# Kernel optimization log

Hardware: AMD Instinct MI355X
Metric: run time of the kernel (lower is better)

## Reference

```python
import jax, jax.numpy as jnp
import numpy as np

N_NODES = 50000
N_EDGES = 800000
D = 128


def _gcn_norm(edge_index, edge_weights, n_nodes):
    # PyG gcn_norm with add_self_loops=True, fill_value=1.0
    src = jnp.concatenate([edge_index[0], jnp.arange(n_nodes)])
    dst = jnp.concatenate([edge_index[1], jnp.arange(n_nodes)])
    w = jnp.concatenate([edge_weights, jnp.ones((n_nodes,), edge_weights.dtype)])
    deg = jax.ops.segment_sum(w, dst, num_segments=n_nodes)
    dinv = jnp.where(deg > 0, jax.lax.rsqrt(deg), 0.0)
    norm = dinv[src] * w * dinv[dst]  # [E + N]
    return src, dst, norm


def _gcn_conv(x, src, dst, norm, W, b, n_nodes):
    h = x @ W                                   # [N, F_out]
    msg = h[src] * norm[:, None]                # gather + scale, [E+N, F_out]
    out = jax.ops.segment_sum(msg, dst, num_segments=n_nodes)
    return out + b


def setup_inputs() -> dict:
    key = jax.random.key(0)
    ks = jax.random.split(key, 12)
    s = 1.0 / np.sqrt(D)
    return {
        "x": jax.random.normal(ks[0], (N_NODES, D), jnp.float32),
        "edge_index": jax.random.randint(ks[1], (2, N_EDGES), 0, N_NODES, jnp.int64),
        "edge_weights": jax.random.uniform(ks[2], (N_EDGES,), jnp.float32),
        "W1": jax.random.normal(ks[3], (D, D), jnp.float32) * s,
        "b1": jnp.zeros((D,), jnp.float32),
        "W2": jax.random.normal(ks[4], (D, D), jnp.float32) * s,
        "b2": jnp.zeros((D,), jnp.float32),
        "W3": jax.random.normal(ks[5], (D, D), jnp.float32) * s,
        "b3": jnp.zeros((D,), jnp.float32),
        "Wl": jax.random.normal(ks[6], (D, D), jnp.float32) * s,
        "bl": jnp.zeros((D,), jnp.float32),
    }


def reference(x, edge_index, edge_weights, W1, b1, W2, b2, W3, b3, Wl, bl):
    n = x.shape[0]
    src, dst, norm = _gcn_norm(edge_index, edge_weights, n)
    h = _gcn_conv(x, src, dst, norm, W1, b1, n)
    h = jax.nn.relu(h)
    h = _gcn_conv(h, src, dst, norm, W2, b2, n)
    h = jax.nn.relu(h)
    h = _gcn_conv(h, src, dst, norm, W3, b3, n)
    # final 'linear' activation entry == nn.Linear(out_size, out_size)
    return h @ Wl + bl
```

## Files before the change

### kernel.cpp

```cpp
#include <hip/hip_runtime.h>
#include <hip/hip_fp16.h>


#define D 128

typedef __attribute__((ext_vector_type(8))) _Float16 half8;
typedef __attribute__((ext_vector_type(4))) float floatx4;

#define CNT_STRIDE 16

__global__ __launch_bounds__(256) void k_edge_pass1(const int* __restrict__ dst,
                                                    unsigned int* __restrict__ cntp,
                                                    int* __restrict__ loc, int E) {
    int e = blockIdx.x * 256 + threadIdx.x;
    if (e < E) {
        int d = dst[e];
        loc[e] = (int)atomicAdd(&cntp[(size_t)d * CNT_STRIDE], 1u);
    }
}

__device__ inline int block_exscan_256(int v) {
    int tid = threadIdx.x;
    int lane = tid & 63, wv = tid >> 6;
    int incl = v;
#pragma unroll
    for (int d = 1; d < 64; d <<= 1) {
        int n = __shfl_up(incl, d, 64);
        if (lane >= d) incl += n;
    }
    __shared__ int wsum[4];
    if (lane == 63) wsum[wv] = incl;
    __syncthreads();
    int woff = 0;
#pragma unroll
    for (int j = 0; j < 4; j++) woff += (j < wv) ? wsum[j] : 0;
    return woff + incl - v;
}

__global__ __launch_bounds__(256) void k_scan_a(const unsigned int* __restrict__ cntp,
                                                int* bsum, int N) {
    int i = blockIdx.x * 256 + threadIdx.x;
    int v = (i < N) ? (int)cntp[(size_t)i * CNT_STRIDE] : 0;
#pragma unroll
    for (int d = 32; d; d >>= 1) v += __shfl_down(v, d, 64);
    __shared__ int ws4[4];
    int lane = threadIdx.x & 63, wv = threadIdx.x >> 6;
    if (lane == 0) ws4[wv] = v;
    __syncthreads();
    if (threadIdx.x == 0) bsum[blockIdx.x] = ws4[0] + ws4[1] + ws4[2] + ws4[3];
}

__global__ __launch_bounds__(256) void k_scan_b(const int* __restrict__ bsum,
                                                int* boff, int nb) {
    int tid = threadIdx.x;
    int v = (tid < nb) ? bsum[tid] : 0;
    int ex = block_exscan_256(v);
    if (tid < nb) boff[tid] = ex;
}

__global__ __launch_bounds__(256) void k_scan_c(const unsigned int* __restrict__ cntp,
                                                const int* __restrict__ boff,
                                                int* rp, int N, int E) {
    int i = blockIdx.x * 256 + threadIdx.x;
    int v = (i < N) ? (int)cntp[(size_t)i * CNT_STRIDE] : 0;
    int ex = block_exscan_256(v);
    if (i < N) rp[i] = boff[blockIdx.x] + ex;
    if (i == 0) rp[N] = E;
}

__global__ __launch_bounds__(256) void k_fill(const int* __restrict__ ei,
                                              const float* __restrict__ w,
                                              const int* __restrict__ rp,
                                              const int* __restrict__ loc,
                                              unsigned int* __restrict__ ev, int E) {
    int e = blockIdx.x * 256 + threadIdx.x;
    if (e < E) {
        int s = ei[e];
        int d = ei[E + e];
        int p = rp[d] + loc[e];
        unsigned int wq = (unsigned int)__float2uint_rn(w[e] * 32767.0f);
        ev[p] = (wq << 17) | (unsigned int)s;
    }
}

__global__ __launch_bounds__(256) void k_deg(const int* __restrict__ rp,
                                             const unsigned int* __restrict__ ev,
                                             float* __restrict__ dinv, int N) {
    int i = blockIdx.x * 256 + threadIdx.x;
    if (i < N) {
        int e0 = rp[i], e1 = rp[i + 1];
        float s = 0.f;
        for (int e = e0; e < e1; e++)
            s += (float)(ev[e] >> 17);
        dinv[i] = rsqrtf(1.0f + s * (1.0f / 32767.0f));
    }
}

template <bool A_IS_F32>
__global__ __launch_bounds__(256) void k_gemm_mfma(const void* __restrict__ Aptr,
                                                   const float* __restrict__ W,
                                                   const float* __restrict__ dinv,
                                                   const float* __restrict__ bias,
                                                   float* __restrict__ C32,
                                                   __half* __restrict__ C16, int N) {
    __shared__ _Float16 Wl[128][136];
    int tid = threadIdx.x;

#pragma unroll
    for (int j = 0; j < 64; j++) {
        int e = tid + j * 256;
        int k = e >> 7, n = e & 127;
        Wl[n][k] = (_Float16)W[e];
    }
    __syncthreads();

    int wave = tid >> 6, lane = tid & 63;
    int m = lane & 15, q = lane >> 4;
    int R0 = blockIdx.x * 128 + wave * 32;

    const float*  A32p = (const float*)Aptr;
    const __half* A16p = (const __half*)Aptr;

    floatx4 acc[2][8];
#pragma unroll
    for (int rt = 0; rt < 2; rt++)
#pragma unroll
        for (int ct = 0; ct < 8; ct++) acc[rt][ct] = (floatx4){0.f, 0.f, 0.f, 0.f};

#pragma unroll
    for (int kk = 0; kk < 4; kk++) {
        half8 a[2];
#pragma unroll
        for (int rt = 0; rt < 2; rt++) {
            int row = R0 + rt * 16 + m;
            half8 t = {0, 0, 0, 0, 0, 0, 0, 0};
            if (row < N) {
                if (A_IS_F32) {
                    const float* p = &A32p[(size_t)row * 128 + kk * 32 + q * 8];
                    float4 f0 = *(const float4*)p;
                    float4 f1 = *(const float4*)(p + 4);
                    t[0] = (_Float16)f0.x; t[1] = (_Float16)f0.y;
                    t[2] = (_Float16)f0.z; t[3] = (_Float16)f0.w;
                    t[4] = (_Float16)f1.x; t[5] = (_Float16)f1.y;
                    t[6] = (_Float16)f1.z; t[7] = (_Float16)f1.w;
                } else {
                    t = *(const half8*)&A16p[(size_t)row * 128 + kk * 32 + q * 8];
                }
            }
            a[rt] = t;
        }
#pragma unroll
        for (int ct = 0; ct < 8; ct++) {
            half8 b = *(const half8*)&Wl[ct * 16 + m][kk * 32 + q * 8];
            acc[0][ct] = __builtin_amdgcn_mfma_f32_16x16x32_f16(a[0], b, acc[0][ct], 0, 0, 0);
            acc[1][ct] = __builtin_amdgcn_mfma_f32_16x16x32_f16(a[1], b, acc[1][ct], 0, 0, 0);
        }
    }

#pragma unroll
    for (int rt = 0; rt < 2; rt++) {
#pragma unroll
        for (int r = 0; r < 4; r++) {
            int row = R0 + rt * 16 + q * 4 + r;
            if (row >= N) continue;
            float dv = (dinv != nullptr) ? dinv[row] : 1.0f;
#pragma unroll
            for (int ct = 0; ct < 8; ct++) {
                int col = ct * 16 + m;
                float v = acc[rt][ct][r] * dv;
                if (C16) C16[(size_t)row * 128 + col] = __float2half_rn(v);
                if (C32) C32[(size_t)row * 128 + col] = v + bias[col];
            }
        }
    }
}

__global__ __launch_bounds__(256) void k_agg(const __half* __restrict__ y16,
                                             const int* __restrict__ rp,
                                             const unsigned int* __restrict__ ev,
                                             const float* __restrict__ dinv,
                                             const float* __restrict__ bias,
                                             __half* __restrict__ out16,
                                             int N, int relu) {
    int i = blockIdx.x * 4 + (threadIdx.x >> 6);
    if (i >= N) return;
    int lane = threadIdx.x & 63;
    int g = lane >> 4;
    int sl = lane & 15;

    float acc[8];
#pragma unroll
    for (int j = 0; j < 8; j++) acc[j] = 0.f;

    int e0 = rp[i], e1 = rp[i + 1];

    for (int e = e0; e < e1; e += 16) {
        unsigned int p[4];
        float v[4];
        uint4 q[4];
#pragma unroll
        for (int u = 0; u < 4; u++) {
            int idx = e + u * 4 + g;
            bool ok = idx < e1;
            p[u] = ev[ok ? idx : e0];
            v[u] = ok ? (float)(p[u] >> 17) * (1.0f / 32767.0f) : 0.0f;
        }
#pragma unroll
        for (int u = 0; u < 4; u++)
            q[u] = *(const uint4*)&y16[(size_t)(p[u] & 0x1FFFFu) * D + sl * 8];
#pragma unroll
        for (int u = 0; u < 4; u++) {
            union { uint4 uu; __half2 h2[4]; } U; U.uu = q[u];
            float2 f0 = __half22float2(U.h2[0]);
            float2 f1 = __half22float2(U.h2[1]);
            float2 f2 = __half22float2(U.h2[2]);
            float2 f3 = __half22float2(U.h2[3]);
            acc[0] = fmaf(v[u], f0.x, acc[0]); acc[1] = fmaf(v[u], f0.y, acc[1]);
            acc[2] = fmaf(v[u], f1.x, acc[2]); acc[3] = fmaf(v[u], f1.y, acc[3]);
            acc[4] = fmaf(v[u], f2.x, acc[4]); acc[5] = fmaf(v[u], f2.y, acc[5]);
            acc[6] = fmaf(v[u], f3.x, acc[6]); acc[7] = fmaf(v[u], f3.y, acc[7]);
        }
    }

#pragma unroll
    for (int j = 0; j < 8; j++) {
        acc[j] += __shfl_xor(acc[j], 16, 64);
        acc[j] += __shfl_xor(acc[j], 32, 64);
    }

    if (g == 0) {
        float di = dinv[i];
        union { uint4 u; __half2 h2[4]; } S;
        S.u = *(const uint4*)&y16[(size_t)i * D + sl * 8];
        float2 s0 = __half22float2(S.h2[0]);
        float2 s1 = __half22float2(S.h2[1]);
        float2 s2 = __half22float2(S.h2[2]);
        float2 s3 = __half22float2(S.h2[3]);
        float4 b0 = *(const float4*)&bias[sl * 8];
        float4 b1 = *(const float4*)&bias[sl * 8 + 4];
        float o[8];
        o[0] = b0.x + di * (acc[0] + s0.x);
        o[1] = b0.y + di * (acc[1] + s0.y);
        o[2] = b0.z + di * (acc[2] + s1.x);
        o[3] = b0.w + di * (acc[3] + s1.y);
        o[4] = b1.x + di * (acc[4] + s2.x);
        o[5] = b1.y + di * (acc[5] + s2.y);
        o[6] = b1.z + di * (acc[6] + s3.x);
        o[7] = b1.w + di * (acc[7] + s3.y);
        if (relu) {
#pragma unroll
            for (int j = 0; j < 8; j++) o[j] = fmaxf(o[j], 0.f);
        }
        union { uint4 u; __half2 h2[4]; } O;
        O.h2[0] = __float22half2_rn(make_float2(o[0], o[1]));
        O.h2[1] = __float22half2_rn(make_float2(o[2], o[3]));
        O.h2[2] = __float22half2_rn(make_float2(o[4], o[5]));
        O.h2[3] = __float22half2_rn(make_float2(o[6], o[7]));
        *(uint4*)&out16[(size_t)i * D + sl * 8] = O.u;
    }
}

extern "C" void kernel_launch(void* const* d_in, const int* in_sizes, int n_in,
                              void* d_out, int out_size, void* d_ws, size_t ws_size,
                              hipStream_t stream) {
    const float* x  = (const float*)d_in[0];
    const int*   ei = (const int*)d_in[1];
    const float* ew = (const float*)d_in[2];
    const float* W1 = (const float*)d_in[3];
    const float* b1 = (const float*)d_in[4];
    const float* W2 = (const float*)d_in[5];
    const float* b2 = (const float*)d_in[6];
    const float* W3 = (const float*)d_in[7];
    const float* b3 = (const float*)d_in[8];
    const float* Wl = (const float*)d_in[9];
    const float* bl = (const float*)d_in[10];

    int N = in_sizes[0] / D;
    int E = in_sizes[2];

    char* ws = (char*)d_ws;
    size_t off = 0;
    auto alloc = [&](size_t bytes) {
        void* p = ws + off;
        off = (off + bytes + 255) & ~(size_t)255;
        return p;
    };
    unsigned int* cntp = (unsigned int*)alloc((size_t)N * CNT_STRIDE * 4);
    float*  dinv = (float*)alloc((size_t)N * 4);
    int*    bsum = (int*)  alloc(1024);
    int*    boff = (int*)  alloc(1024);
    int*    rp   = (int*)  alloc((size_t)(N + 1) * 4);
    int*    loc  = (int*)  alloc((size_t)E * 4);
    unsigned int* ev = (unsigned int*)alloc((size_t)E * 4);
    __half* y16  = (__half*)alloc((size_t)N * D * 2);
    __half* z16  = (__half*)alloc((size_t)N * D * 2);

    int nbN = (N + 255) / 256;
    int nbE = (E + 255) / 256;

    hipMemsetAsync(cntp, 0, (size_t)N * CNT_STRIDE * 4, stream);
    k_edge_pass1<<<nbE, 256, 0, stream>>>(ei + E, cntp, loc, E);
    k_scan_a<<<nbN, 256, 0, stream>>>(cntp, bsum, N);
    k_scan_b<<<1, 256, 0, stream>>>(bsum, boff, nbN);
    k_scan_c<<<nbN, 256, 0, stream>>>(cntp, boff, rp, N, E);
    k_fill<<<nbE, 256, 0, stream>>>(ei, ew, rp, loc, ev, E);
    k_deg<<<nbN, 256, 0, stream>>>(rp, ev, dinv, N);

    int gg = (N + 127) / 128;
    int ga = (N + 3) / 4;

    k_gemm_mfma<true ><<<gg, 256, 0, stream>>>(x,   W1, dinv, nullptr, nullptr, y16, N);
    k_agg<<<ga, 256, 0, stream>>>(y16, rp, ev, dinv, b1, z16, N, 1);
    k_gemm_mfma<false><<<gg, 256, 0, stream>>>(z16, W2, dinv, nullptr, nullptr, y16, N);
    k_agg<<<ga, 256, 0, stream>>>(y16, rp, ev, dinv, b2, z16, N, 1);
    k_gemm_mfma<false><<<gg, 256, 0, stream>>>(z16, W3, dinv, nullptr, nullptr, y16, N);
    k_agg<<<ga, 256, 0, stream>>>(y16, rp, ev, dinv, b3, z16, N, 0);
    k_gemm_mfma<false><<<gg, 256, 0, stream>>>(z16, Wl, nullptr, bl, (float*)d_out, nullptr, N);
}
```

Baseline: 300.8 us.

## Fuse first GEMM with edge counting and fold full GCN norm into edges

The first-layer GEMM and the per-edge destination counting now run in one launch, using disjoint block ranges. The count uses a packed 64-bit atomic that accumulates both the edge count and the quantized weight, so the degree comes straight out of the scan and the separate degree kernel is gone. The fill kernel stores the full symmetric norm w*dinv[s]*dinv[d] in each edge word. That lets the GEMM epilogues drop the per-row dinv scaling, and aggregation only scales the self term by dinv squared. The cost is 64-bit atomics on a wider padded counter array, and the norm product is now quantized to 15 bits instead of the raw weight.

New measurement: 285.6 us. 5.1% less time.

```diff
diff --git a/kernel.cpp b/kernel.cpp
--- a/kernel.cpp
+++ b/kernel.cpp
@@ -3,106 +3,15 @@
 
 
 #define D 128
+#define CNT64_STRIDE 8
 
 typedef __attribute__((ext_vector_type(8))) _Float16 half8;
 typedef __attribute__((ext_vector_type(4))) float floatx4;
 
-#define CNT_STRIDE 16
-
-__global__ __launch_bounds__(256) void k_edge_pass1(const int* __restrict__ dst,
-                                                    unsigned int* __restrict__ cntp,
-                                                    int* __restrict__ loc, int E) {
-    int e = blockIdx.x * 256 + threadIdx.x;
-    if (e < E) {
-        int d = dst[e];
-        loc[e] = (int)atomicAdd(&cntp[(size_t)d * CNT_STRIDE], 1u);
-    }
-}
-
-__device__ inline int block_exscan_256(int v) {
-    int tid = threadIdx.x;
-    int lane = tid & 63, wv = tid >> 6;
-    int incl = v;
-#pragma unroll
-    for (int d = 1; d < 64; d <<= 1) {
-        int n = __shfl_up(incl, d, 64);
-        if (lane >= d) incl += n;
-    }
-    __shared__ int wsum[4];
-    if (lane == 63) wsum[wv] = incl;
-    __syncthreads();
-    int woff = 0;
-#pragma unroll
-    for (int j = 0; j < 4; j++) woff += (j < wv) ? wsum[j] : 0;
-    return woff + incl - v;
-}
-
-__global__ __launch_bounds__(256) void k_scan_a(const unsigned int* __restrict__ cntp,
-                                                int* bsum, int N) {
-    int i = blockIdx.x * 256 + threadIdx.x;
-    int v = (i < N) ? (int)cntp[(size_t)i * CNT_STRIDE] : 0;
-#pragma unroll
-    for (int d = 32; d; d >>= 1) v += __shfl_down(v, d, 64);
-    __shared__ int ws4[4];
-    int lane = threadIdx.x & 63, wv = threadIdx.x >> 6;
-    if (lane == 0) ws4[wv] = v;
-    __syncthreads();
-    if (threadIdx.x == 0) bsum[blockIdx.x] = ws4[0] + ws4[1] + ws4[2] + ws4[3];
-}
-
-__global__ __launch_bounds__(256) void k_scan_b(const int* __restrict__ bsum,
-                                                int* boff, int nb) {
-    int tid = threadIdx.x;
-    int v = (tid < nb) ? bsum[tid] : 0;
-    int ex = block_exscan_256(v);
-    if (tid < nb) boff[tid] = ex;
-}
-
-__global__ __launch_bounds__(256) void k_scan_c(const unsigned int* __restrict__ cntp,
-                                                const int* __restrict__ boff,
-                                                int* rp, int N, int E) {
-    int i = blockIdx.x * 256 + threadIdx.x;
-    int v = (i < N) ? (int)cntp[(size_t)i * CNT_STRIDE] : 0;
-    int ex = block_exscan_256(v);
-    if (i < N) rp[i] = boff[blockIdx.x] + ex;
-    if (i == 0) rp[N] = E;
-}
-
-__global__ __launch_bounds__(256) void k_fill(const int* __restrict__ ei,
-                                              const float* __restrict__ w,
-                                              const int* __restrict__ rp,
-                                              const int* __restrict__ loc,
-                                              unsigned int* __restrict__ ev, int E) {
-    int e = blockIdx.x * 256 + threadIdx.x;
-    if (e < E) {
-        int s = ei[e];
-        int d = ei[E + e];
-        int p = rp[d] + loc[e];
-        unsigned int wq = (unsigned int)__float2uint_rn(w[e] * 32767.0f);
-        ev[p] = (wq << 17) | (unsigned int)s;
-    }
-}
-
-__global__ __launch_bounds__(256) void k_deg(const int* __restrict__ rp,
-                                             const unsigned int* __restrict__ ev,
-                                             float* __restrict__ dinv, int N) {
-    int i = blockIdx.x * 256 + threadIdx.x;
-    if (i < N) {
-        int e0 = rp[i], e1 = rp[i + 1];
-        float s = 0.f;
-        for (int e = e0; e < e1; e++)
-            s += (float)(ev[e] >> 17);
-        dinv[i] = rsqrtf(1.0f + s * (1.0f / 32767.0f));
-    }
-}
-
 template <bool A_IS_F32>
-__global__ __launch_bounds__(256) void k_gemm_mfma(const void* __restrict__ Aptr,
-                                                   const float* __restrict__ W,
-                                                   const float* __restrict__ dinv,
-                                                   const float* __restrict__ bias,
-                                                   float* __restrict__ C32,
-                                                   __half* __restrict__ C16, int N) {
+__device__ __forceinline__ void gemm_body(int bid, const void* Aptr,
+                                          const float* W, const float* bias,
+                                          float* C32, __half* C16, int N) {
     __shared__ _Float16 Wl[128][136];
     int tid = threadIdx.x;
 
@@ -116,7 +25,7 @@
 
     int wave = tid >> 6, lane = tid & 63;
     int m = lane & 15, q = lane >> 4;
-    int R0 = blockIdx.x * 128 + wave * 32;
+    int R0 = bid * 128 + wave * 32;
 
     const float*  A32p = (const float*)Aptr;
     const __half* A16p = (const __half*)Aptr;
@@ -163,15 +72,115 @@
         for (int r = 0; r < 4; r++) {
             int row = R0 + rt * 16 + q * 4 + r;
             if (row >= N) continue;
-            float dv = (dinv != nullptr) ? dinv[row] : 1.0f;
 #pragma unroll
             for (int ct = 0; ct < 8; ct++) {
                 int col = ct * 16 + m;
-                float v = acc[rt][ct][r] * dv;
+                float v = acc[rt][ct][r];
                 if (C16) C16[(size_t)row * 128 + col] = __float2half_rn(v);
                 if (C32) C32[(size_t)row * 128 + col] = v + bias[col];
             }
         }
+    }
+}
+
+template <bool A_IS_F32>
+__global__ __launch_bounds__(256) void k_gemm_mfma(const void* __restrict__ Aptr,
+                                                   const float* __restrict__ W,
+                                                   const float* __restrict__ bias,
+                                                   float* __restrict__ C32,
+                                                   __half* __restrict__ C16, int N) {
+    gemm_body<A_IS_F32>(blockIdx.x, Aptr, W, bias, C32, C16, N);
+}
+
+__global__ __launch_bounds__(256) void k_build_gemm1(const float* __restrict__ x,
+                                                     const float* __restrict__ W1,
+                                                     __half* __restrict__ y16,
+                                                     const int* __restrict__ dst,
+                                                     const float* __restrict__ w,
+                                                     unsigned long long* __restrict__ cnt8,
+                                                     int* __restrict__ loc,
+                                                     int N, int E, int gg) {
+    if ((int)blockIdx.x < gg) {
+        gemm_body<true>(blockIdx.x, x, W1, nullptr, nullptr, y16, N);
+        return;
+    }
+    int e = ((int)blockIdx.x - gg) * 256 + threadIdx.x;
+    if (e < E) {
+        int d = dst[e];
+        unsigned int wq = __float2uint_rn(w[e] * 32767.0f);
+        unsigned long long old =
+            atomicAdd(&cnt8[(size_t)d * CNT64_STRIDE], (1ull << 32) | (unsigned long long)wq);
+        loc[e] = (int)(old >> 32);
+    }
+}
+
+__device__ inline int block_exscan_256(int v) {
+    int tid = threadIdx.x;
+    int lane = tid & 63, wv = tid >> 6;
+    int incl = v;
+#pragma unroll
+    for (int d = 1; d < 64; d <<= 1) {
+        int n = __shfl_up(incl, d, 64);
+        if (lane >= d) incl += n;
+    }
+    __shared__ int wsum[4];
+    if (lane == 63) wsum[wv] = incl;
+    __syncthreads();
+    int woff = 0;
+#pragma unroll
+    for (int j = 0; j < 4; j++) woff += (j < wv) ? wsum[j] : 0;
+    return woff + incl - v;
+}
+
+__global__ __launch_bounds__(256) void k_scan_a(const unsigned long long* __restrict__ cnt8,
+                                                int* bsum, int N) {
+    int i = blockIdx.x * 256 + threadIdx.x;
+    int v = (i < N) ? (int)(cnt8[(size_t)i * CNT64_STRIDE] >> 32) : 0;
+#pragma unroll
+    for (int d = 32; d; d >>= 1) v += __shfl_down(v, d, 64);
+    __shared__ int ws4[4];
+    int lane = threadIdx.x & 63, wv = threadIdx.x >> 6;
+    if (lane == 0) ws4[wv] = v;
+    __syncthreads();
+    if (threadIdx.x == 0) bsum[blockIdx.x] = ws4[0] + ws4[1] + ws4[2] + ws4[3];
+}
+
+__global__ __launch_bounds__(256) void k_scan_b(const int* __restrict__ bsum,
+                                                int* boff, int nb) {
+    int tid = threadIdx.x;
+    int v = (tid < nb) ? bsum[tid] : 0;
+    int ex = block_exscan_256(v);
+    if (tid < nb) boff[tid] = ex;
+}
+
+__global__ __launch_bounds__(256) void k_scan_c(const unsigned long long* __restrict__ cnt8,
+                                                const int* __restrict__ boff,
+                                                int* rp, float* dinv, int N, int E) {
+    int i = blockIdx.x * 256 + threadIdx.x;
+    unsigned long long p = (i < N) ? cnt8[(size_t)i * CNT64_STRIDE] : 0ull;
+    int v = (int)(p >> 32);
+    int ex = block_exscan_256(v);
+    if (i < N) {
+        rp[i] = boff[blockIdx.x] + ex;
+        dinv[i] = rsqrtf(1.0f + (float)(unsigned int)p * (1.0f / 32767.0f));
+    }
+    if (i == 0) rp[N] = E;
+}
+
+__global__ __launch_bounds__(256) void k_fill(const int* __restrict__ ei,
+                                              const float* __restrict__ w,
+                                              const float* __restrict__ dinv,
+                                              const int* __restrict__ rp,
+                                              const int* __restrict__ loc,
+                                              unsigned int* __restrict__ ev, int E) {
+    int e = blockIdx.x * 256 + threadIdx.x;
+    if (e < E) {
+        int s = ei[e];
+        int d = ei[E + e];
+        int p = rp[d] + loc[e];
+        float val = w[e] * dinv[s] * dinv[d];
+        unsigned int wq = __float2uint_rn(val * 32767.0f);
+        ev[p] = (wq << 17) | (unsigned int)s;
     }
 }
 
@@ -230,6 +239,7 @@
 
     if (g == 0) {
         float di = dinv[i];
+        float di2 = di * di;
         union { uint4 u; __half2 h2[4]; } S;
         S.u = *(const uint4*)&y16[(size_t)i * D + sl * 8];
         float2 s0 = __half22float2(S.h2[0]);
@@ -239,14 +249,14 @@
         float4 b0 = *(const float4*)&bias[sl * 8];
         float4 b1 = *(const float4*)&bias[sl * 8 + 4];
         float o[8];
-        o[0] = b0.x + di * (acc[0] + s0.x);
-        o[1] = b0.y + di * (acc[1] + s0.y);
-        o[2] = b0.z + di * (acc[2] + s1.x);
-        o[3] = b0.w + di * (acc[3] + s1.y);
-        o[4] = b1.x + di * (acc[4] + s2.x);
-        o[5] = b1.y + di * (acc[5] + s2.y);
-        o[6] = b1.z + di * (acc[6] + s3.x);
-        o[7] = b1.w + di * (acc[7] + s3.y);
+        o[0] = b0.x + acc[0] + di2 * s0.x;
+        o[1] = b0.y + acc[1] + di2 * s0.y;
+        o[2] = b0.z + acc[2] + di2 * s1.x;
+        o[3] = b0.w + acc[3] + di2 * s1.y;
+        o[4] = b1.x + acc[4] + di2 * s2.x;
+        o[5] = b1.y + acc[5] + di2 * s2.y;
+        o[6] = b1.z + acc[6] + di2 * s3.x;
+        o[7] = b1.w + acc[7] + di2 * s3.y;
         if (relu) {
 #pragma unroll
             for (int j = 0; j < 8; j++) o[j] = fmaxf(o[j], 0.f);
@@ -285,7 +295,7 @@
         off = (off + bytes + 255) & ~(size_t)255;
         return p;
     };
-    unsigned int* cntp = (unsigned int*)alloc((size_t)N * CNT_STRIDE * 4);
+    unsigned long long* cnt8 = (unsigned long long*)alloc((size_t)N * 64);
     float*  dinv = (float*)alloc((size_t)N * 4);
     int*    bsum = (int*)  alloc(1024);
     int*    boff = (int*)  alloc(1024);
@@ -297,23 +307,21 @@
 
     int nbN = (N + 255) / 256;
     int nbE = (E + 255) / 256;
-
-    hipMemsetAsync(cntp, 0, (size_t)N * CNT_STRIDE * 4, stream);
-    k_edge_pass1<<<nbE, 256, 0, stream>>>(ei + E, cntp, loc, E);
-    k_scan_a<<<nbN, 256, 0, stream>>>(cntp, bsum, N);
+    int gg  = (N + 127) / 128;
+    int ga  = (N + 3) / 4;
+
+    hipMemsetAsync(cnt8, 0, (size_t)N * 64, stream);
+    k_build_gemm1<<<gg + nbE, 256, 0, stream>>>(x, W1, y16, ei + E, ew,
+                                                cnt8, loc, N, E, gg);
+    k_scan_a<<<nbN, 256, 0, stream>>>(cnt8, bsum, N);
     k_scan_b<<<1, 256, 0, stream>>>(bsum, boff, nbN);
-    k_scan_c<<<nbN, 256, 0, stream>>>(cntp, boff, rp, N, E);
-    k_fill<<<nbE, 256, 0, stream>>>(ei, ew, rp, loc, ev, E);
-    k_deg<<<nbN, 256, 0, stream>>>(rp, ev, dinv, N);
-
-    int gg = (N + 127) / 128;
-    int ga = (N + 3) / 4;
-
-    k_gemm_mfma<true ><<<gg, 256, 0, stream>>>(x,   W1, dinv, nullptr, nullptr, y16, N);
+    k_scan_c<<<nbN, 256, 0, stream>>>(cnt8, boff, rp, dinv, N, E);
+    k_fill<<<nbE, 256, 0, stream>>>(ei, ew, dinv, rp, loc, ev, E);
+
     k_agg<<<ga, 256, 0, stream>>>(y16, rp, ev, dinv, b1, z16, N, 1);
-    k_gemm_mfma<false><<<gg, 256, 0, stream>>>(z16, W2, dinv, nullptr, nullptr, y16, N);
+    k_gemm_mfma<false><<<gg, 256, 0, stream>>>(z16, W2, nullptr, nullptr, y16, N);
     k_agg<<<ga, 256, 0, stream>>>(y16, rp, ev, dinv, b2, z16, N, 1);
-    k_gemm_mfma<false><<<gg, 256, 0, stream>>>(z16, W3, dinv, nullptr, nullptr, y16, N);
+    k_gemm_mfma<false><<<gg, 256, 0, stream>>>(z16, W3, nullptr, nullptr, y16, N);
     k_agg<<<ga, 256, 0, stream>>>(y16, rp, ev, dinv, b3, z16, N, 0);
-    k_gemm_mfma<false><<<gg, 256, 0, stream>>>(z16, Wl, nullptr, bl, (float*)d_out, nullptr, N);
-}
+    k_gemm_mfma<false><<<gg, 256, 0, stream>>>(z16, Wl, bl, (float*)d_out, nullptr, N);
+}
```
